# Optimization experiments

Measured on AMD Instinct MI355X. Metric: run time of the kernel, lower is better.

Reference implementation:

```python
import jax, jax.numpy as jnp
import numpy as np

NH, KD, HD = 8, 32, 32          # n_heads, qk dim, value dim per head
D = NH * HD                     # 256 channels (v.reshape requires d == nh*hd)
SCALE = 0.17677669529663687     # kd ** -0.5


def setup_inputs() -> dict:
    key = jax.random.key(0)
    k1, k2 = jax.random.split(key)
    x = jax.random.normal(k1, (2, D, 64, 64), dtype=jnp.float32)
    # dp[1]: bias-free 1x1 conv D -> NH*(4*KD+HD) = 1280, fan-in scaled
    w_proj = jax.random.normal(k2, (NH * (4 * KD + HD), D), dtype=jnp.float32) * np.float32(1.0 / np.sqrt(D))
    return {"x": x, "w_proj": w_proj}


def reference(x, w_proj):
    b, d, h, w = x.shape
    # dp[0] = Identity; dp[1] = 1x1 conv as a channel matmul
    p = jnp.einsum('bchw,oc->bohw', x, w_proj).reshape(b, NH, 4 * KD + HD, h, w)
    rq = p[:, :, 0 * KD:1 * KD]
    rk = p[:, :, 1 * KD:2 * KD]
    cq = p[:, :, 2 * KD:3 * KD]
    ck = p[:, :, 3 * KD:4 * KD]
    v = p[:, :, 4 * KD:]                      # (b, NH, HD, h, w)
    # row attention over h (independently per column w), softmax over i (dim 2)
    r = jax.nn.softmax(jnp.einsum('bHdiw,bHdjw->bHijw', rq, rk) * SCALE, axis=2)
    # column attention over w (independently per row h), softmax over i (dim 2)
    c = jax.nn.softmax(jnp.einsum('bHdhi,bHdhj->bHihj', cq, ck) * SCALE, axis=2)
    # trilinear combine: out[b,H,d,h,w] = sum_{i,j} r[b,H,i,h,w] * v[b,H,d,i,j] * c[b,H,j,h,w]
    # contract v with c first, then with r (intermediate m is (b,NH,HD,h,h,w))
    m = jnp.einsum('bHdij,bHjhw->bHdihw', v, c)
    out = jnp.einsum('bHihw,bHdihw->bHdhw', r, m).reshape(b, d, h, w)
    # residual: dp[2] = Identity, dp[3] = Identity
    return out + v.reshape(b, d, h, w)
```

## Files before the change

kernel.cpp:

```cpp
#include <hip/hip_runtime.h>
#include <stdint.h>


#define SCALE 0.17677669529663687f
typedef unsigned short ushort_t;
typedef __attribute__((ext_vector_type(8))) short bf16x8;
typedef __attribute__((ext_vector_type(4))) float f32x4;

__device__ __forceinline__ unsigned short f2bf(float f) {
  unsigned int b = __float_as_uint(f);
  b += 0x7fffu + ((b >> 16) & 1u);
  return (unsigned short)(b >> 16);
}
__device__ __forceinline__ float bflo(unsigned int u) { return __uint_as_float(u << 16); }
__device__ __forceinline__ float bfhi(unsigned int u) { return __uint_as_float(u & 0xffff0000u); }
__device__ __forceinline__ unsigned int pk2(float a, float b) {
  return (unsigned int)f2bf(a) | ((unsigned int)f2bf(b) << 16);
}
__device__ __forceinline__ f32x4 mfma16(bf16x8 a, bf16x8 b, f32x4 c) {
  return __builtin_amdgcn_mfma_f32_16x16x32_bf16(a, b, c, 0, 0, 0);
}
__device__ __forceinline__ void gld16(const void* g, void* l) {
  __builtin_amdgcn_global_load_lds(
      (const __attribute__((address_space(1))) unsigned int*)g,
      (__attribute__((address_space(3))) unsigned int*)l, 16, 0, 0);
}

__global__ __launch_bounds__(256) void prep(const float* __restrict__ x,
                                            const float* __restrict__ w,
                                            ushort_t* __restrict__ xtf,
                                            ushort_t* __restrict__ wf) {
  const int bid = blockIdx.x;
  const int t = threadIdx.x;
  if (bid < 512) {
    __shared__ float tile[128][33];
    const int b = bid >> 8, rem = bid & 255;
    const int kc = rem >> 5;
    const int n0 = (rem & 31) * 128;
    const float* xb = x + (size_t)b * 256 * 4096;
#pragma unroll
    for (int rep = 0; rep < 4; rep++) {
      int idx = rep * 256 + t;
      int kk = idx >> 5, nn4 = (idx & 31) * 4;
      float4 f = *(const float4*)&xb[(size_t)(kc * 32 + kk) * 4096 + n0 + nn4];
      tile[nn4 + 0][kk] = f.x; tile[nn4 + 1][kk] = f.y;
      tile[nn4 + 2][kk] = f.z; tile[nn4 + 3][kk] = f.w;
    }
    __syncthreads();
    ushort_t* xo = xtf + (size_t)b * 1048576;
#pragma unroll
    for (int rep = 0; rep < 2; rep++) {
      int idx = rep * 256 + t;
      int n = idx >> 2, k8 = (idx & 3) * 8;
      uint4 o;
      o.x = pk2(tile[n][k8 + 0], tile[n][k8 + 1]);
      o.y = pk2(tile[n][k8 + 2], tile[n][k8 + 3]);
      o.z = pk2(tile[n][k8 + 4], tile[n][k8 + 5]);
      o.w = pk2(tile[n][k8 + 6], tile[n][k8 + 7]);
      int nt = (n0 + n) >> 4;
      int lane = ((n0 + n) & 15) + ((k8 >> 3) << 4);
      *(uint4*)&xo[(size_t)((nt * 8 + kc) * 64 + lane) * 8] = o;
    }
  } else {
    const int mt = bid - 512;
    const int wv = t >> 6, l = t & 63;
#pragma unroll
    for (int s = 0; s < 2; s++) {
      int kc = wv + s * 4;
      const float* src = &w[(size_t)(mt * 16 + (l & 15)) * 256 + kc * 32 + (l >> 4) * 8];
      float4 f0 = *(const float4*)&src[0];
      float4 f1 = *(const float4*)&src[4];
      uint4 o;
      o.x = pk2(f0.x, f0.y); o.y = pk2(f0.z, f0.w);
      o.z = pk2(f1.x, f1.y); o.w = pk2(f1.z, f1.w);
      *(uint4*)&wf[(size_t)((mt * 8 + kc) * 64 + l) * 8] = o;
    }
  }
}

__global__ __launch_bounds__(256, 4) void proj_mfma_v3(const ushort_t* __restrict__ wf,
                                                       const ushort_t* __restrict__ xtf,
                                                       ushort_t* __restrict__ Qr,
                                                       ushort_t* __restrict__ Kr,
                                                       ushort_t* __restrict__ Qc,
                                                       ushort_t* __restrict__ Kc,
                                                       float* __restrict__ P_v) {
  const int b = blockIdx.z, by = blockIdx.y, bx = blockIdx.x;
  const int m0 = by * 128, n0 = bx * 128;
  const int t = threadIdx.x, wv = t >> 6, l = t & 63;
  const int row = l & 15, quad = l >> 4;
  const int wm = wv >> 1, wn = wv & 1;
  const ushort_t* xb = xtf + (size_t)b * 1048576;

  f32x4 acc[4][4];
#pragma unroll
  for (int i = 0; i < 4; i++)
#pragma unroll
    for (int j = 0; j < 4; j++) acc[i][j] = (f32x4){0.f, 0.f, 0.f, 0.f};

  const size_t abase = (size_t)(by * 8 + wm * 4) * 4096 + l * 8;
  const size_t bbase = (size_t)(bx * 8 + wn * 4) * 4096 + l * 8;

  for (int kc = 0; kc < 8; kc++) {
    bf16x8 af[4], bfr[4];
#pragma unroll
    for (int mf = 0; mf < 4; mf++)
      af[mf] = *(const bf16x8*)&wf[abase + mf * 4096 + kc * 512];
#pragma unroll
    for (int nf = 0; nf < 4; nf++)
      bfr[nf] = *(const bf16x8*)&xb[bbase + nf * 4096 + kc * 512];
#pragma unroll
    for (int mf = 0; mf < 4; mf++)
#pragma unroll
      for (int nf = 0; nf < 4; nf++)
        acc[mf][nf] = mfma16(af[mf], bfr[nf], acc[mf][nf]);
  }

#pragma unroll
  for (int mf = 0; mf < 4; mf++) {
    int mb = m0 + wm * 64 + mf * 16 + quad * 4;
    int H = mb / 160;
    int rem = mb - H * 160;
    int sec = rem >> 5;
    int d0 = rem & 31;
    int bh = b * 8 + H;
    if (sec < 4) {
      ushort_t* base = (sec == 0) ? Qr : (sec == 1) ? Kr : (sec == 2) ? Qc : Kc;
      base += (size_t)bh * 131072;
#pragma unroll
      for (int nf = 0; nf < 4; nf++) {
        int n = n0 + wn * 64 + nf * 16 + row;
        int orow = (sec < 2) ? ((n & 63) * 64 + (n >> 6)) : n;
        uint2 o;
        o.x = pk2(acc[mf][nf][0], acc[mf][nf][1]);
        o.y = pk2(acc[mf][nf][2], acc[mf][nf][3]);
        *(uint2*)&base[(size_t)orow * 32 + d0] = o;
      }
    } else {
      float* pvb = P_v + ((size_t)bh * 32 + d0) * 4096;
#pragma unroll
      for (int nf = 0; nf < 4; nf++) {
        int n = n0 + wn * 64 + nf * 16 + row;
#pragma unroll
        for (int r = 0; r < 4; r++)
          pvb[(size_t)r * 4096 + n] = acc[mf][nf][r];
      }
    }
  }
}

__global__ __launch_bounds__(256) void mid(const ushort_t* __restrict__ Qr,
                                           const ushort_t* __restrict__ Kr,
                                           const ushort_t* __restrict__ Qc,
                                           const ushort_t* __restrict__ Kc,
                                           ushort_t* __restrict__ Rs,
                                           ushort_t* __restrict__ Cs,
                                           const float* __restrict__ P_v,
                                           ushort_t* __restrict__ vf) {
  __shared__ float tile[8][64][33];
  const int bid = blockIdx.x;
  const int t = threadIdx.x, wv = t >> 6, l = t & 63;
  if (bid < 512) {
    const int mode = bid >> 8;
    const int idx = bid & 255;
    const int bh = idx >> 4, gq = idx & 15;
    const int col = l & 15, quad = l >> 4;
    const int g = gq * 4 + wv;
    const ushort_t* Qb = (mode ? Qc : Qr) + (size_t)bh * 131072 + (size_t)g * 2048;
    const ushort_t* Kb = (mode ? Kc : Kr) + (size_t)bh * 131072 + (size_t)g * 2048;

    bf16x8 aq[4], bk[4];
#pragma unroll
    for (int f = 0; f < 4; f++) {
      aq[f] = *(const bf16x8*)&Qb[(size_t)(f * 16 + col) * 32 + quad * 8];
      bk[f] = *(const bf16x8*)&Kb[(size_t)(f * 16 + col) * 32 + quad * 8];
    }
    f32x4 s[4][4];
#pragma unroll
    for (int i0 = 0; i0 < 4; i0++)
#pragma unroll
      for (int j0 = 0; j0 < 4; j0++)
        s[i0][j0] = mfma16(aq[i0], bk[j0], (f32x4){0.f, 0.f, 0.f, 0.f});

    ushort_t* ob = (mode ? Cs : Rs) + (size_t)bh * 262144;
#pragma unroll
    for (int j0 = 0; j0 < 4; j0++) {
      float sv[16];
#pragma unroll
      for (int i0 = 0; i0 < 4; i0++)
#pragma unroll
        for (int r = 0; r < 4; r++) sv[i0 * 4 + r] = s[i0][j0][r] * SCALE;
      float mx = sv[0];
#pragma unroll
      for (int q = 1; q < 16; q++) mx = fmaxf(mx, sv[q]);
      mx = fmaxf(mx, __shfl_xor(mx, 16));
      mx = fmaxf(mx, __shfl_xor(mx, 32));
      float e[16], sum = 0.f;
#pragma unroll
      for (int q = 0; q < 16; q++) { e[q] = __expf(sv[q] - mx); sum += e[q]; }
      sum += __shfl_xor(sum, 16);
      sum += __shfl_xor(sum, 32);
      const float inv = 1.f / sum;
      const int j = j0 * 16 + col;
#pragma unroll
      for (int i0 = 0; i0 < 4; i0++) {
        uint2 o;
        o.x = pk2(e[i0 * 4 + 0] * inv, e[i0 * 4 + 1] * inv);
        o.y = pk2(e[i0 * 4 + 2] * inv, e[i0 * 4 + 3] * inv);
        size_t addr = mode ? ((size_t)(g * 64 + j) * 64 + i0 * 16 + quad * 4)
                           : ((size_t)(j * 64 + g) * 64 + i0 * 16 + quad * 4);
        *(uint2*)&ob[addr] = o;
      }
    }
  } else {
    const int vid = bid - 512;
    const int jc = vid & 7, bh = vid >> 3;
    const int j0 = jc * 8;
    const float* pvb = P_v + (size_t)bh * 131072;
#pragma unroll
    for (int rep = 0; rep < 8; rep++) {
      int idx = rep * 256 + t;
      int d = idx >> 6, i = idx & 63;
      float4 f0 = *(const float4*)&pvb[(size_t)d * 4096 + i * 64 + j0];
      float4 f1 = *(const float4*)&pvb[(size_t)d * 4096 + i * 64 + j0 + 4];
      tile[0][i][d] = f0.x; tile[1][i][d] = f0.y;
      tile[2][i][d] = f0.z; tile[3][i][d] = f0.w;
      tile[4][i][d] = f1.x; tile[5][i][d] = f1.y;
      tile[6][i][d] = f1.z; tile[7][i][d] = f1.w;
    }
    __syncthreads();
    ushort_t* vo = vf + (size_t)bh * 131072;
    const int fid = t >> 6;
    const int d = (fid & 1) * 16 + (l & 15);
    const int i0 = (fid >> 1) * 32 + (l >> 4) * 8;
#pragma unroll
    for (int rep = 0; rep < 8; rep++) {
      int jl = rep;
      uint4 o;
      o.x = pk2(tile[jl][i0 + 0][d], tile[jl][i0 + 1][d]);
      o.y = pk2(tile[jl][i0 + 2][d], tile[jl][i0 + 3][d]);
      o.z = pk2(tile[jl][i0 + 4][d], tile[jl][i0 + 5][d]);
      o.w = pk2(tile[jl][i0 + 6][d], tile[jl][i0 + 7][d]);
      *(uint4*)&vo[(size_t)(((j0 + jl) * 4 + fid) * 64 + l) * 8] = o;
    }
  }
}

__global__ __launch_bounds__(256, 2) void attn_apply_v5(const float* __restrict__ P_v,
                                                        const ushort_t* __restrict__ rs,
                                                        const ushort_t* __restrict__ cs,
                                                        const ushort_t* __restrict__ vf,
                                                        float* __restrict__ out) {
  __shared__ ushort_t buf[2][8192];
  const int bid = blockIdx.x;
  const int ds = bid & 1, pg = (bid >> 1) & 15, bh = bid >> 5;
  const int b = bh >> 3, H = bh & 7;
  const int t = threadIdx.x, wv = t >> 6, l = t & 63;
  const int row = l & 15, quad = l >> 4;
  const int h = pg * 4 + wv;
  const ushort_t* rsl = rs + (size_t)bh * 262144 + (size_t)h * 4096;
  const ushort_t* csl = cs + (size_t)bh * 262144 + (size_t)h * 4096;
  const ushort_t* vb = vf + (size_t)bh * 131072;

  bf16x8 rf[2][4];
#pragma unroll
  for (int nf = 0; nf < 4; nf++)
#pragma unroll
    for (int kc = 0; kc < 2; kc++)
      rf[kc][nf] = *(const bf16x8*)&rsl[(size_t)(nf * 16 + row) * 64 + kc * 32 + quad * 8];

  f32x4 acc[4];
#pragma unroll
  for (int nf = 0; nf < 4; nf++) acc[nf] = (f32x4){0.f, 0.f, 0.f, 0.f};

#pragma unroll
  for (int u = 0; u < 4; u++) {
    int idx = u * 256 + t;
    int jj = idx >> 7, kcl = (idx >> 6) & 1, ll = idx & 63;
    gld16(&vb[(size_t)((jj * 4 + ds + 2 * kcl) * 64 + ll) * 8], &buf[0][idx * 8]);
  }
  __syncthreads();

  for (int ph = 0; ph < 8; ph++) {
    const ushort_t* bcur = buf[ph & 1];
    if (ph < 7) {
#pragma unroll
      for (int u = 0; u < 4; u++) {
        int idx = u * 256 + t;
        int jj = idx >> 7, kcl = (idx >> 6) & 1, ll = idx & 63;
        gld16(&vb[(size_t)(((ph + 1) * 8 + jj) * 4 + ds + 2 * kcl) * 64 * 8 + ll * 8],
              &buf[(ph + 1) & 1][idx * 8]);
      }
    }
    float cv[8][4];
#pragma unroll
    for (int nf = 0; nf < 4; nf++) {
      uint4 u = *(const uint4*)&csl[(size_t)(nf * 16 + row) * 64 + ph * 8];
      cv[0][nf] = bflo(u.x); cv[1][nf] = bfhi(u.x);
      cv[2][nf] = bflo(u.y); cv[3][nf] = bfhi(u.y);
      cv[4][nf] = bflo(u.z); cv[5][nf] = bfhi(u.z);
      cv[6][nf] = bflo(u.w); cv[7][nf] = bfhi(u.w);
    }
#pragma unroll
    for (int jj = 0; jj < 8; jj++) {
      bf16x8 a0 = *(const bf16x8*)&bcur[((jj * 2 + 0) * 64 + l) * 8];
      bf16x8 a1 = *(const bf16x8*)&bcur[((jj * 2 + 1) * 64 + l) * 8];
#pragma unroll
      for (int nf = 0; nf < 4; nf++) {
        f32x4 tt = (f32x4){0.f, 0.f, 0.f, 0.f};
        tt = mfma16(a0, rf[0][nf], tt);
        tt = mfma16(a1, rf[1][nf], tt);
        acc[nf] += tt * cv[jj][nf];
      }
    }
    __syncthreads();
  }

  const float* pv = P_v + (size_t)bh * 131072 + h * 64;
  float* ob = out + ((size_t)b * 256 + H * 32) * 4096 + h * 64;
#pragma unroll
  for (int nf = 0; nf < 4; nf++)
#pragma unroll
    for (int reg = 0; reg < 4; reg++) {
      int d = ds * 16 + quad * 4 + reg;
      int wc = nf * 16 + row;
      ob[(size_t)d * 4096 + wc] = acc[nf][reg] + pv[(size_t)d * 4096 + wc];
    }
}

extern "C" void kernel_launch(void* const* d_in, const int* in_sizes, int n_in,
                              void* d_out, int out_size, void* d_ws, size_t ws_size,
                              hipStream_t stream) {
  const float* x = (const float*)d_in[0];
  const float* w = (const float*)d_in[1];
  float* out = (float*)d_out;
  float* ws = (float*)d_ws;
  float* P_v = ws;
  ushort_t* Rs  = (ushort_t*)(ws + 2097152);
  ushort_t* Cs  = (ushort_t*)(ws + 4194304);
  ushort_t* Vf  = (ushort_t*)(ws + 6291456);
  ushort_t* Qr  = (ushort_t*)(ws + 7340032);
  ushort_t* Kr  = (ushort_t*)(ws + 8388608);
  ushort_t* Qc  = (ushort_t*)(ws + 9437184);
  ushort_t* Kc  = (ushort_t*)(ws + 10485760);
  ushort_t* Wf  = (ushort_t*)(ws + 11534336);
  ushort_t* Xtf = (ushort_t*)(ws + 11698176);

  prep<<<592, 256, 0, stream>>>(x, w, Xtf, Wf);
  proj_mfma_v3<<<dim3(32, 10, 2), 256, 0, stream>>>(Wf, Xtf, Qr, Kr, Qc, Kc, P_v);
  mid<<<640, 256, 0, stream>>>(Qr, Kr, Qc, Kc, Rs, Cs, P_v, Vf);
  attn_apply_v5<<<512, 256, 0, stream>>>(P_v, Rs, Cs, Vf, out);
}
```

Before: 122.7 us.

## Store V projection as bf16, remap blocks by XCD, deepen apply staging

The V section of the projection is now written as bf16 instead of fp32. This halves the traffic for the V transpose in mid and for the residual read in attn_apply, and drops the float-to-bf16 repacking in mid. Block indices in mid and attn_apply are remapped so that consecutive block IDs spread across 8 (b,head) groups, which is meant to place blocks that share data on the same XCD L2. attn_apply also stages 16 j-columns per phase with doubled LDS buffers, using 4 phases instead of 8. The cost is that the residual V is now rounded to bf16, which loses accuracy, and the larger LDS buffers may lower occupancy.

```diff
diff --git a/kernel.cpp b/kernel.cpp
--- a/kernel.cpp
+++ b/kernel.cpp
@@ -78,13 +78,13 @@
   }
 }
 
-__global__ __launch_bounds__(256, 4) void proj_mfma_v3(const ushort_t* __restrict__ wf,
+__global__ __launch_bounds__(256, 4) void proj_mfma_v4(const ushort_t* __restrict__ wf,
                                                        const ushort_t* __restrict__ xtf,
                                                        ushort_t* __restrict__ Qr,
                                                        ushort_t* __restrict__ Kr,
                                                        ushort_t* __restrict__ Qc,
                                                        ushort_t* __restrict__ Kc,
-                                                       float* __restrict__ P_v) {
+                                                       ushort_t* __restrict__ P_vb) {
   const int b = blockIdx.z, by = blockIdx.y, bx = blockIdx.x;
   const int m0 = by * 128, n0 = bx * 128;
   const int t = threadIdx.x, wv = t >> 6, l = t & 63;
@@ -137,13 +137,13 @@
         *(uint2*)&base[(size_t)orow * 32 + d0] = o;
       }
     } else {
-      float* pvb = P_v + ((size_t)bh * 32 + d0) * 4096;
+      ushort_t* pvb = P_vb + ((size_t)bh * 32 + d0) * 4096;
 #pragma unroll
       for (int nf = 0; nf < 4; nf++) {
         int n = n0 + wn * 64 + nf * 16 + row;
 #pragma unroll
         for (int r = 0; r < 4; r++)
-          pvb[(size_t)r * 4096 + n] = acc[mf][nf][r];
+          pvb[(size_t)r * 4096 + n] = f2bf(acc[mf][nf][r]);
       }
     }
   }
@@ -155,15 +155,15 @@
                                            const ushort_t* __restrict__ Kc,
                                            ushort_t* __restrict__ Rs,
                                            ushort_t* __restrict__ Cs,
-                                           const float* __restrict__ P_v,
+                                           const ushort_t* __restrict__ P_vb,
                                            ushort_t* __restrict__ vf) {
-  __shared__ float tile[8][64][33];
+  __shared__ ushort_t tile[8][64][34];
   const int bid = blockIdx.x;
   const int t = threadIdx.x, wv = t >> 6, l = t & 63;
   if (bid < 512) {
-    const int mode = bid >> 8;
-    const int idx = bid & 255;
-    const int bh = idx >> 4, gq = idx & 15;
+    const int xr = bid & 7, rest = bid >> 3;
+    const int gq = rest & 15, mode = (rest >> 4) & 1, bhHi = rest >> 5;
+    const int bh = bhHi * 8 + xr;
     const int col = l & 15, quad = l >> 4;
     const int g = gq * 4 + wv;
     const ushort_t* Qb = (mode ? Qc : Qr) + (size_t)bh * 131072 + (size_t)g * 2048;
@@ -213,20 +213,24 @@
       }
     }
   } else {
-    const int vid = bid - 512;
-    const int jc = vid & 7, bh = vid >> 3;
+    const int v = bid - 512;
+    const int xr = v & 7, jc = (v >> 3) & 7, bhHi = v >> 6;
+    const int bh = bhHi * 8 + xr;
     const int j0 = jc * 8;
-    const float* pvb = P_v + (size_t)bh * 131072;
+    const ushort_t* pvb = P_vb + (size_t)bh * 131072;
 #pragma unroll
     for (int rep = 0; rep < 8; rep++) {
       int idx = rep * 256 + t;
       int d = idx >> 6, i = idx & 63;
-      float4 f0 = *(const float4*)&pvb[(size_t)d * 4096 + i * 64 + j0];
-      float4 f1 = *(const float4*)&pvb[(size_t)d * 4096 + i * 64 + j0 + 4];
-      tile[0][i][d] = f0.x; tile[1][i][d] = f0.y;
-      tile[2][i][d] = f0.z; tile[3][i][d] = f0.w;
-      tile[4][i][d] = f1.x; tile[5][i][d] = f1.y;
-      tile[6][i][d] = f1.z; tile[7][i][d] = f1.w;
+      uint4 u = *(const uint4*)&pvb[(size_t)d * 4096 + i * 64 + j0];
+      tile[0][i][d] = (ushort_t)(u.x & 0xffff);
+      tile[1][i][d] = (ushort_t)(u.x >> 16);
+      tile[2][i][d] = (ushort_t)(u.y & 0xffff);
+      tile[3][i][d] = (ushort_t)(u.y >> 16);
+      tile[4][i][d] = (ushort_t)(u.z & 0xffff);
+      tile[5][i][d] = (ushort_t)(u.z >> 16);
+      tile[6][i][d] = (ushort_t)(u.w & 0xffff);
+      tile[7][i][d] = (ushort_t)(u.w >> 16);
     }
     __syncthreads();
     ushort_t* vo = vf + (size_t)bh * 131072;
@@ -234,26 +238,27 @@
     const int d = (fid & 1) * 16 + (l & 15);
     const int i0 = (fid >> 1) * 32 + (l >> 4) * 8;
 #pragma unroll
-    for (int rep = 0; rep < 8; rep++) {
-      int jl = rep;
+    for (int jl = 0; jl < 8; jl++) {
       uint4 o;
-      o.x = pk2(tile[jl][i0 + 0][d], tile[jl][i0 + 1][d]);
-      o.y = pk2(tile[jl][i0 + 2][d], tile[jl][i0 + 3][d]);
-      o.z = pk2(tile[jl][i0 + 4][d], tile[jl][i0 + 5][d]);
-      o.w = pk2(tile[jl][i0 + 6][d], tile[jl][i0 + 7][d]);
+      o.x = (unsigned int)tile[jl][i0 + 0][d] | ((unsigned int)tile[jl][i0 + 1][d] << 16);
+      o.y = (unsigned int)tile[jl][i0 + 2][d] | ((unsigned int)tile[jl][i0 + 3][d] << 16);
+      o.z = (unsigned int)tile[jl][i0 + 4][d] | ((unsigned int)tile[jl][i0 + 5][d] << 16);
+      o.w = (unsigned int)tile[jl][i0 + 6][d] | ((unsigned int)tile[jl][i0 + 7][d] << 16);
       *(uint4*)&vo[(size_t)(((j0 + jl) * 4 + fid) * 64 + l) * 8] = o;
     }
   }
 }
 
-__global__ __launch_bounds__(256, 2) void attn_apply_v5(const float* __restrict__ P_v,
+__global__ __launch_bounds__(256, 2) void attn_apply_v6(const ushort_t* __restrict__ P_vb,
                                                         const ushort_t* __restrict__ rs,
                                                         const ushort_t* __restrict__ cs,
                                                         const ushort_t* __restrict__ vf,
                                                         float* __restrict__ out) {
-  __shared__ ushort_t buf[2][8192];
+  __shared__ ushort_t buf[2][16384];
   const int bid = blockIdx.x;
-  const int ds = bid & 1, pg = (bid >> 1) & 15, bh = bid >> 5;
+  const int xr = bid & 7, rest = bid >> 3;
+  const int ds = rest & 1, pg = (rest >> 1) & 15, bhHi = rest >> 5;
+  const int bh = bhHi * 8 + xr;
   const int b = bh >> 3, H = bh & 7;
   const int t = threadIdx.x, wv = t >> 6, l = t & 63;
   const int row = l & 15, quad = l >> 4;
@@ -274,35 +279,40 @@
   for (int nf = 0; nf < 4; nf++) acc[nf] = (f32x4){0.f, 0.f, 0.f, 0.f};
 
 #pragma unroll
-  for (int u = 0; u < 4; u++) {
+  for (int u = 0; u < 8; u++) {
     int idx = u * 256 + t;
     int jj = idx >> 7, kcl = (idx >> 6) & 1, ll = idx & 63;
     gld16(&vb[(size_t)((jj * 4 + ds + 2 * kcl) * 64 + ll) * 8], &buf[0][idx * 8]);
   }
   __syncthreads();
 
-  for (int ph = 0; ph < 8; ph++) {
+  for (int ph = 0; ph < 4; ph++) {
     const ushort_t* bcur = buf[ph & 1];
-    if (ph < 7) {
-#pragma unroll
-      for (int u = 0; u < 4; u++) {
+    if (ph < 3) {
+#pragma unroll
+      for (int u = 0; u < 8; u++) {
         int idx = u * 256 + t;
         int jj = idx >> 7, kcl = (idx >> 6) & 1, ll = idx & 63;
-        gld16(&vb[(size_t)(((ph + 1) * 8 + jj) * 4 + ds + 2 * kcl) * 64 * 8 + ll * 8],
+        gld16(&vb[(size_t)((((ph + 1) * 16 + jj) * 4 + ds + 2 * kcl) * 64 + ll) * 8],
               &buf[(ph + 1) & 1][idx * 8]);
       }
     }
-    float cv[8][4];
+    float cv[16][4];
 #pragma unroll
     for (int nf = 0; nf < 4; nf++) {
-      uint4 u = *(const uint4*)&csl[(size_t)(nf * 16 + row) * 64 + ph * 8];
-      cv[0][nf] = bflo(u.x); cv[1][nf] = bfhi(u.x);
-      cv[2][nf] = bflo(u.y); cv[3][nf] = bfhi(u.y);
-      cv[4][nf] = bflo(u.z); cv[5][nf] = bfhi(u.z);
-      cv[6][nf] = bflo(u.w); cv[7][nf] = bfhi(u.w);
-    }
-#pragma unroll
-    for (int jj = 0; jj < 8; jj++) {
+      uint4 u0 = *(const uint4*)&csl[(size_t)(nf * 16 + row) * 64 + ph * 16];
+      uint4 u1 = *(const uint4*)&csl[(size_t)(nf * 16 + row) * 64 + ph * 16 + 8];
+      cv[0][nf] = bflo(u0.x);  cv[1][nf] = bfhi(u0.x);
+      cv[2][nf] = bflo(u0.y);  cv[3][nf] = bfhi(u0.y);
+      cv[4][nf] = bflo(u0.z);  cv[5][nf] = bfhi(u0.z);
+      cv[6][nf] = bflo(u0.w);  cv[7][nf] = bfhi(u0.w);
+      cv[8][nf] = bflo(u1.x);  cv[9][nf] = bfhi(u1.x);
+      cv[10][nf] = bflo(u1.y); cv[11][nf] = bfhi(u1.y);
+      cv[12][nf] = bflo(u1.z); cv[13][nf] = bfhi(u1.z);
+      cv[14][nf] = bflo(u1.w); cv[15][nf] = bfhi(u1.w);
+    }
+#pragma unroll
+    for (int jj = 0; jj < 16; jj++) {
       bf16x8 a0 = *(const bf16x8*)&bcur[((jj * 2 + 0) * 64 + l) * 8];
       bf16x8 a1 = *(const bf16x8*)&bcur[((jj * 2 + 1) * 64 + l) * 8];
 #pragma unroll
@@ -316,7 +326,7 @@
     __syncthreads();
   }
 
-  const float* pv = P_v + (size_t)bh * 131072 + h * 64;
+  const ushort_t* pv = P_vb + (size_t)bh * 131072 + h * 64;
   float* ob = out + ((size_t)b * 256 + H * 32) * 4096 + h * 64;
 #pragma unroll
   for (int nf = 0; nf < 4; nf++)
@@ -324,7 +334,8 @@
     for (int reg = 0; reg < 4; reg++) {
       int d = ds * 16 + quad * 4 + reg;
       int wc = nf * 16 + row;
-      ob[(size_t)d * 4096 + wc] = acc[nf][reg] + pv[(size_t)d * 4096 + wc];
+      ob[(size_t)d * 4096 + wc] =
+          acc[nf][reg] + bflo((unsigned int)pv[(size_t)d * 4096 + wc]);
     }
 }
 
@@ -335,19 +346,19 @@
   const float* w = (const float*)d_in[1];
   float* out = (float*)d_out;
   float* ws = (float*)d_ws;
-  float* P_v = ws;
-  ushort_t* Rs  = (ushort_t*)(ws + 2097152);
-  ushort_t* Cs  = (ushort_t*)(ws + 4194304);
-  ushort_t* Vf  = (ushort_t*)(ws + 6291456);
-  ushort_t* Qr  = (ushort_t*)(ws + 7340032);
-  ushort_t* Kr  = (ushort_t*)(ws + 8388608);
-  ushort_t* Qc  = (ushort_t*)(ws + 9437184);
-  ushort_t* Kc  = (ushort_t*)(ws + 10485760);
-  ushort_t* Wf  = (ushort_t*)(ws + 11534336);
-  ushort_t* Xtf = (ushort_t*)(ws + 11698176);
+  ushort_t* P_vb = (ushort_t*)ws;
+  ushort_t* Rs  = (ushort_t*)(ws + 1048576);
+  ushort_t* Cs  = (ushort_t*)(ws + 3145728);
+  ushort_t* Vf  = (ushort_t*)(ws + 5242880);
+  ushort_t* Qr  = (ushort_t*)(ws + 6291456);
+  ushort_t* Kr  = (ushort_t*)(ws + 7340032);
+  ushort_t* Qc  = (ushort_t*)(ws + 8388608);
+  ushort_t* Kc  = (ushort_t*)(ws + 9437184);
+  ushort_t* Wf  = (ushort_t*)(ws + 10485760);
+  ushort_t* Xtf = (ushort_t*)(ws + 10649600);
 
   prep<<<592, 256, 0, stream>>>(x, w, Xtf, Wf);
-  proj_mfma_v3<<<dim3(32, 10, 2), 256, 0, stream>>>(Wf, Xtf, Qr, Kr, Qc, Kc, P_v);
-  mid<<<640, 256, 0, stream>>>(Qr, Kr, Qc, Kc, Rs, Cs, P_v, Vf);
-  attn_apply_v5<<<512, 256, 0, stream>>>(P_v, Rs, Cs, Vf, out);
-}
+  proj_mfma_v4<<<dim3(32, 10, 2), 256, 0, stream>>>(Wf, Xtf, Qr, Kr, Qc, Kc, P_vb);
+  mid<<<640, 256, 0, stream>>>(Qr, Kr, Qc, Kc, Rs, Cs, P_vb, Vf);
+  attn_apply_v6<<<512, 256, 0, stream>>>(P_vb, Rs, Cs, Vf, out);
+}
```

After: 114.9 us. -6.3%, faster.
